# Performance work log

Hardware: AMD Instinct MI355X
Metric: run time of the kernel (lower is better)

The kernel has to match this reference:

```python
import jax, jax.numpy as jnp
import numpy as np

B, C, Ci, H, W = 8, 256, 128, 64, 64
EPS = 1e-5


def conv1x1(x, w, b):
    # x: [B,C,H,W], w: [O,C], b: [O] -> [B,O,H,W]
    return jnp.einsum('bchw,oc->bohw', x, w) + b[None, :, None, None]


def maxpool2(x):
    b, c, h, w = x.shape
    return x.reshape(b, c, h // 2, 2, w // 2, 2).max(axis=(3, 5))


def setup_inputs() -> dict:
    key = jax.random.key(0)
    ks = jax.random.split(key, 12)
    s_in = 1.0 / np.sqrt(C)
    s_ic = 1.0 / np.sqrt(Ci)
    return {
        'x': jax.random.normal(ks[0], (B, C, H, W), dtype=jnp.float32),
        'g_w': jax.random.normal(ks[1], (Ci, C), dtype=jnp.float32) * s_in,
        'g_b': jax.random.normal(ks[2], (Ci,), dtype=jnp.float32) * 0.01,
        'theta_w': jax.random.normal(ks[3], (Ci, C), dtype=jnp.float32) * s_in,
        'theta_b': jax.random.normal(ks[4], (Ci,), dtype=jnp.float32) * 0.01,
        'phi_w': jax.random.normal(ks[5], (Ci, C), dtype=jnp.float32) * s_in,
        'phi_b': jax.random.normal(ks[6], (Ci,), dtype=jnp.float32) * 0.01,
        'W_w': jax.random.normal(ks[7], (C, Ci), dtype=jnp.float32) * s_ic,
        'W_b': jax.random.normal(ks[8], (C,), dtype=jnp.float32) * 0.01,
        'bn_gamma': jax.random.normal(ks[9], (C,), dtype=jnp.float32) * 0.1 + 1.0,
        'bn_beta': jax.random.normal(ks[10], (C,), dtype=jnp.float32) * 0.1,
        'bn_mean': jnp.zeros((C,), dtype=jnp.float32),
        'bn_var': jax.random.uniform(ks[11], (C,), dtype=jnp.float32) * 0.5 + 0.75,
    }


def reference(x, g_w, g_b, theta_w, theta_b, phi_w, phi_b, W_w, W_b, bn_gamma, bn_beta, bn_mean, bn_var):
    b = x.shape[0]
    # g and phi: 1x1 conv then 2x2 max-pool (sub_sample=True)
    g_x = maxpool2(conv1x1(x, g_w, g_b)).reshape(b, Ci, -1)          # [B,Ci,Np]
    g_x = jnp.transpose(g_x, (0, 2, 1))                               # [B,Np,Ci]
    theta_x = conv1x1(x, theta_w, theta_b).reshape(b, Ci, -1)         # [B,Ci,N]
    theta_x = jnp.transpose(theta_x, (0, 2, 1))                       # [B,N,Ci]
    phi_x = maxpool2(conv1x1(x, phi_w, phi_b)).reshape(b, Ci, -1)     # [B,Ci,Np]
    f = jnp.einsum('bnc,bcm->bnm', theta_x, phi_x)                    # [B,N,Np]
    f_div_C = jax.nn.softmax(f, axis=-1)                              # embedded_gaussian: plain softmax, no scaling
    y = jnp.einsum('bnm,bmc->bnc', f_div_C, g_x)                      # [B,N,Ci]
    y = jnp.transpose(y, (0, 2, 1)).reshape(b, Ci, H, W)              # [B,Ci,H,W]
    # W: 1x1 conv + BatchNorm (inference form with running stats)
    W_y = conv1x1(y, W_w, W_b)
    inv = bn_gamma / jnp.sqrt(bn_var + EPS)
    W_y = (W_y - bn_mean[None, :, None, None]) * inv[None, :, None, None] + bn_beta[None, :, None, None]
    return W_y + x
```

## Files before the change

### kernel.cpp

```cpp
#include <hip/hip_runtime.h>
#include <math.h>

#define Bn   8
#define Cc   256
#define Cin  128
#define Hh   64
#define Ww   64
#define Nn   4096
#define Npl  1024
#define EPSf 1e-5f

typedef __attribute__((ext_vector_type(8))) short    short8;
typedef __attribute__((ext_vector_type(8))) _Float16 half8;
typedef __attribute__((ext_vector_type(4))) float    floatx4;

__device__ __forceinline__ unsigned short f2bf(float f) {
    unsigned int u = __float_as_uint(f);
    u += 0x7fffu + ((u >> 16) & 1u);
    return (unsigned short)(u >> 16);
}
__device__ __forceinline__ unsigned short f2h(float f) {
    _Float16 h = (_Float16)f;
    return __builtin_bit_cast(unsigned short, h);
}
__device__ __forceinline__ float h2f(unsigned short u) {
    return (float)__builtin_bit_cast(_Float16, u);
}

__device__ __forceinline__ unsigned int cvtpk_bf16(float lo, float hi) {
    unsigned int r;
    asm("v_cvt_pk_bf16_f32 %0, %1, %2" : "=v"(r) : "v"(lo), "v"(hi));
    return r;
}

__device__ __forceinline__ void gload_lds16(const unsigned short* g, unsigned short* l) {
    __builtin_amdgcn_global_load_lds(
        (const __attribute__((address_space(1))) unsigned int*)g,
        (__attribute__((address_space(3))) unsigned int*)l, 16, 0, 0);
}

__global__ __launch_bounds__(256) void k_prep(
    const float* __restrict__ g_w, const float* __restrict__ th_w,
    const float* __restrict__ ph_w,
    const float* __restrict__ W_w, const float* __restrict__ W_b,
    const float* __restrict__ gamma, const float* __restrict__ beta,
    const float* __restrict__ mean,  const float* __restrict__ var,
    unsigned short* __restrict__ gWh,
    unsigned short* __restrict__ thWh, unsigned short* __restrict__ thWl,
    unsigned short* __restrict__ phWh, unsigned short* __restrict__ phWl,
    unsigned short* __restrict__ Wh, float* __restrict__ cvec)
{
    int i = blockIdx.x * 256 + threadIdx.x;
    if (i < 98304) {
        int seg = i >> 15;
        int idx = i & 32767;
        float v = (seg == 0 ? g_w : (seg == 1 ? th_w : ph_w))[idx];
        unsigned short hi = f2h(v);
        if (seg == 0) gWh[idx] = hi;
        else {
            (seg == 1 ? thWh : phWh)[idx] = hi;
            (seg == 1 ? thWl : phWl)[idx] = f2h(v - h2f(hi));
        }
    } else {
        int j = i - 98304;
        int o = j >> 7;
        float inv = gamma[o] * rsqrtf(var[o] + EPSf);
        Wh[j] = f2h(W_w[j] * inv);
        if (j < Cc) {
            float invi = gamma[j] * rsqrtf(var[j] + EPSf);
            cvec[j] = (W_b[j] - mean[j]) * invi + beta[j];
        }
    }
}

#define XPAD 264

__global__ __launch_bounds__(256, 2) void k_conv3(
    const float* __restrict__ x,
    const unsigned short* __restrict__ gWh,
    const unsigned short* __restrict__ thWh, const unsigned short* __restrict__ thWl,
    const unsigned short* __restrict__ phWh, const unsigned short* __restrict__ phWl,
    const float* __restrict__ g_b, const float* __restrict__ th_b,
    const float* __restrict__ ph_b,
    unsigned short* __restrict__ thetaT,
    unsigned short* __restrict__ gPc,
    unsigned short* __restrict__ phiPt)
{
    __shared__ __align__(16) unsigned short Xhi[64 * XPAD];
    __shared__ __align__(16) unsigned short Xlo[64 * XPAD];

    const int t    = threadIdx.x;
    const int w    = t >> 6;
    const int l    = t & 63;
    const int quad = l >> 4;
    const int l16  = l & 15;
    const int b    = blockIdx.x >> 6;
    const int tile = blockIdx.x & 63;
    const int ty   = tile >> 1;
    const int tx   = tile & 1;

    {
        const float4* xg = (const float4*)x;
        unsigned int* XhiW = (unsigned int*)Xhi;
        unsigned int* XloW = (unsigned int*)Xlo;
        #pragma unroll
        for (int it = 0; it < 8; ++it) {
            int idx = t + 256 * it;
            int c2  = idx >> 4;
            int p4  = idx & 15;
            int n   = (2 * ty + (p4 >> 3)) * Ww + tx * 32 + (p4 & 7) * 4;
            float4 va = xg[((size_t)(b * Cc + 2 * c2) * Nn + n) >> 2];
            float4 vb = xg[((size_t)(b * Cc + 2 * c2 + 1) * Nn + n) >> 2];
            const float fa[4] = {va.x, va.y, va.z, va.w};
            const float fb[4] = {vb.x, vb.y, vb.z, vb.w};
            #pragma unroll
            for (int i = 0; i < 4; ++i) {
                int px = p4 * 4 + i;
                unsigned short ha = f2h(fa[i]), hb = f2h(fb[i]);
                unsigned short la = f2h(fa[i] - h2f(ha));
                unsigned short lb = f2h(fb[i] - h2f(hb));
                XhiW[px * 132 + c2] = (unsigned int)ha | ((unsigned int)hb << 16);
                XloW[px * 132 + c2] = (unsigned int)la | ((unsigned int)lb << 16);
            }
        }
    }
    __syncthreads();

    floatx4 acc[6][4] = {};

    #pragma unroll 2
    for (int kd = 0; kd < 8; ++kd) {
        half8 bhi[4], blo[4];
        #pragma unroll
        for (int nt = 0; nt < 4; ++nt) {
            bhi[nt] = *(const half8*)&Xhi[(nt * 16 + l16) * XPAD + kd * 32 + quad * 8];
            blo[nt] = *(const half8*)&Xlo[(nt * 16 + l16) * XPAD + kd * 32 + quad * 8];
        }
        #pragma unroll
        for (int ti = 0; ti < 6; ++ti) {
            int ot  = w + 4 * ti;
            int seg = ot >> 3;
            size_t aoff = (size_t)((ot & 7) * 16 + l16) * Cc + kd * 32 + quad * 8;
            const unsigned short* wh = (seg == 0 ? gWh : (seg == 1 ? thWh : phWh));
            half8 ah = *(const half8*)&wh[aoff];
            #pragma unroll
            for (int nt = 0; nt < 4; ++nt)
                acc[ti][nt] = __builtin_amdgcn_mfma_f32_16x16x32_f16(ah, bhi[nt], acc[ti][nt], 0, 0, 0);
            if (seg != 0) {
                const unsigned short* wl = (seg == 1 ? thWl : phWl);
                half8 al = *(const half8*)&wl[aoff];
                #pragma unroll
                for (int nt = 0; nt < 4; ++nt) {
                    acc[ti][nt] = __builtin_amdgcn_mfma_f32_16x16x32_f16(ah, blo[nt], acc[ti][nt], 0, 0, 0);
                    acc[ti][nt] = __builtin_amdgcn_mfma_f32_16x16x32_f16(al, bhi[nt], acc[ti][nt], 0, 0, 0);
                }
            }
        }
    }

    #pragma unroll
    for (int ti = 0; ti < 6; ++ti) {
        int ot  = w + 4 * ti;
        int seg = ot >> 3;
        int ol  = (ot & 7) * 16 + quad * 4;
        if (seg == 1) {
            float b0 = th_b[ol], b1 = th_b[ol + 1], b2 = th_b[ol + 2], b3 = th_b[ol + 3];
            #pragma unroll
            for (int nt = 0; nt < 4; ++nt) {
                int n = (2 * ty + (nt >> 1)) * Ww + tx * 32 + (nt & 1) * 16 + l16;
                ushort4 v;
                v.x = f2h(acc[ti][nt][0] + b0);
                v.y = f2h(acc[ti][nt][1] + b1);
                v.z = f2h(acc[ti][nt][2] + b2);
                v.w = f2h(acc[ti][nt][3] + b3);
                *(ushort4*)&thetaT[((size_t)b * Nn + n) * Cin + ol] = v;
            }
        } else {
            const float* bb = (seg == 0 ? g_b : ph_b);
            float b0 = bb[ol], b1 = bb[ol + 1], b2 = bb[ol + 2], b3 = bb[ol + 3];
            #pragma unroll
            for (int pp = 0; pp < 2; ++pp) {
                float pm[4];
                #pragma unroll
                for (int r = 0; r < 4; ++r) {
                    float m = fmaxf(acc[ti][pp][r], acc[ti][pp + 2][r]);
                    pm[r] = fmaxf(m, __shfl_xor(m, 1, 64));
                }
                int np = ty * 32 + tx * 16 + pp * 8 + (l16 >> 1);
                if ((l16 & 1) == 0) {
                    if (seg == 0) {
                        gPc[((size_t)b * Cin + ol + 0) * Npl + np] = f2bf(pm[0] + b0);
                        gPc[((size_t)b * Cin + ol + 1) * Npl + np] = f2bf(pm[1] + b1);
                        gPc[((size_t)b * Cin + ol + 2) * Npl + np] = f2bf(pm[2] + b2);
                        gPc[((size_t)b * Cin + ol + 3) * Npl + np] = f2bf(pm[3] + b3);
                    } else {
                        ushort4 v;
                        v.x = f2h(pm[0] + b0); v.y = f2h(pm[1] + b1);
                        v.z = f2h(pm[2] + b2); v.w = f2h(pm[3] + b3);
                        *(ushort4*)&phiPt[((size_t)b * Npl + np) * Cin + ol] = v;
                    }
                }
            }
        }
    }
}

__device__ __forceinline__ void stage_kv(
    unsigned short* smem, int sel, int chg, int b, int grp, int wq,
    int mK, int gK, int cV, int gV,
    const unsigned short* __restrict__ phiPt,
    const unsigned short* __restrict__ gPc)
{
    unsigned short* Kb = smem + sel * 16384;
    if (grp == 0) {
        #pragma unroll
        for (int j = 0; j < 4; ++j) {
            int slot = wq * 4 + j;
            int m  = slot * 4 + mK;
            int gs = gK ^ (m & 7);
            gload_lds16(&phiPt[((size_t)b * Npl + chg * 64 + m) * Cin + gs * 8],
                        &Kb[slot * 512]);
        }
    } else {
        unsigned short* Vb = Kb + 8192;
        #pragma unroll
        for (int j = 0; j < 4; ++j) {
            int slot = wq * 4 + j;
            int c  = slot * 8 + cV;
            int gs = gV ^ (c & 7);
            gload_lds16(&gPc[((size_t)b * Cin + c) * Npl + chg * 64 + gs * 8],
                        &Vb[slot * 512]);
        }
    }
}

#define SSHIFT 20.0f

__global__ __launch_bounds__(512, 4) void k_attn_out(
    const unsigned short* __restrict__ thetaT,
    const unsigned short* __restrict__ phiPt,
    const unsigned short* __restrict__ gPc,
    const unsigned short* __restrict__ Wh,
    const float* __restrict__ cvec,
    const float* __restrict__ x,
    float* __restrict__ out)
{
    __shared__ __align__(16) unsigned short smem[40960];

    const int t    = threadIdx.x;
    const int w    = t >> 6;
    const int wq   = w & 3;
    const int grp  = w >> 2;
    const int l    = t & 63;
    const int quad = l >> 4;
    const int l16  = l & 15;
    const int bid  = blockIdx.x;
    const int wid  = (bid & 7) * 64 + (bid >> 3);
    const int b    = wid >> 6;
    const int qb   = wid & 63;
    const int n0   = qb * 64;

    uint4 qr[4];
    #pragma unroll
    for (int kd = 0; kd < 4; ++kd)
        qr[kd] = *(const uint4*)&thetaT[((size_t)b * Nn + n0 + wq * 16 + l16) * Cin
                                        + kd * 32 + quad * 8];
    #pragma unroll
    for (int kd = 0; kd < 4; ++kd)
        asm volatile("" : "+v"(qr[kd].x), "+v"(qr[kd].y), "+v"(qr[kd].z), "+v"(qr[kd].w));
    half8 qf[4];
    #pragma unroll
    for (int kd = 0; kd < 4; ++kd) qf[kd] = __builtin_bit_cast(half8, qr[kd]);

    floatx4 yacc[8] = {};
    float liq = 0.f;

    const int mK = l >> 4;
    const int gK = l & 15;
    const int cV = l >> 3;
    const int gV = l & 7;

    stage_kv(smem, 0, 0, b, grp, wq, mK, gK, cV, gV, phiPt, gPc);
    asm volatile("s_waitcnt vmcnt(0)" ::: "memory");
    __syncthreads();

    #pragma unroll 2
    for (int ch = 0; ch < 16; ++ch) {
        const int cur = ch & 1;
        if (ch < 15)
            stage_kv(smem, cur ^ 1, ch + 1, b, grp, wq, mK, gK, cV, gV, phiPt, gPc);

        const unsigned short* Ks = smem + cur * 16384;
        const unsigned short* Vt = Ks + 8192;

        floatx4 sacc[2] = {};
        #pragma unroll
        for (int mtl = 0; mtl < 2; ++mtl) {
            int mt = grp * 2 + mtl;
            #pragma unroll
            for (int kd = 0; kd < 4; ++kd) {
                half8 kf = *(const half8*)&Ks[(mt * 16 + l16) * 128
                                              + (((kd * 4 + quad) ^ (l16 & 7)) << 3)];
                sacc[mtl] = __builtin_amdgcn_mfma_f32_16x16x32_f16(kf, qf[kd], sacc[mtl], 0, 0, 0);
            }
        }

        float ex0[4], ex1[4];
        #pragma unroll
        for (int r = 0; r < 4; ++r) {
            ex0[r] = __expf(sacc[0][r] - SSHIFT);
            ex1[r] = __expf(sacc[1][r] - SSHIFT);
            liq += ex0[r] + ex1[r];
        }

        unsigned int a0 = cvtpk_bf16(ex0[0], ex0[1]);
        unsigned int a1 = cvtpk_bf16(ex1[0], ex1[1]);
        unsigned int b0 = cvtpk_bf16(ex0[2], ex0[3]);
        unsigned int b1 = cvtpk_bf16(ex1[2], ex1[3]);
        asm volatile("v_permlane32_swap_b32 %0, %1" : "+v"(a0), "+v"(a1));
        asm volatile("v_permlane16_swap_b32 %0, %1" : "+v"(a0), "+v"(a1));
        asm volatile("v_permlane32_swap_b32 %0, %1" : "+v"(b0), "+v"(b1));
        asm volatile("v_permlane16_swap_b32 %0, %1" : "+v"(b0), "+v"(b1));
        uint4 pw; pw.x = a0; pw.y = b0; pw.z = a1; pw.w = b1;
        short8 pf = __builtin_bit_cast(short8, pw);

        #pragma unroll
        for (int ct = 0; ct < 8; ++ct) {
            short8 vf = *(const short8*)&Vt[(ct * 16 + l16) * 64
                                            + (((grp * 4 + quad) ^ (l16 & 7)) << 3)];
            yacc[ct] = __builtin_amdgcn_mfma_f32_16x16x32_bf16(pf, vf, yacc[ct], 0, 0, 0);
        }

        asm volatile("s_waitcnt vmcnt(0)" ::: "memory");
        __syncthreads();
    }

    liq += __shfl_xor(liq, 16, 64);
    liq += __shfl_xor(liq, 32, 64);

    float* cbuf = (float*)smem;
    const int ci = (wq * 64 + l) * 33;
    if (grp == 1) {
        #pragma unroll
        for (int ct = 0; ct < 8; ++ct)
            #pragma unroll
            for (int r = 0; r < 4; ++r) cbuf[ci + ct * 4 + r] = yacc[ct][r];
        cbuf[ci + 32] = liq;
    }
    __syncthreads();
    if (grp == 0) {
        #pragma unroll
        for (int ct = 0; ct < 8; ++ct)
            #pragma unroll
            for (int r = 0; r < 4; ++r) yacc[ct][r] += cbuf[ci + ct * 4 + r];
        liq += cbuf[ci + 32];
    }
    __syncthreads();

    {
        unsigned short* Ws = smem + 8192;
        #pragma unroll
        for (int j = 0; j < 8; ++j) {
            int slot = w * 8 + j;
            int row  = slot * 4 + mK;
            int gs   = gK ^ (row & 7);
            gload_lds16(&Wh[(size_t)row * Cin + gs * 8], &Ws[slot * 512]);
        }
    }

    if (grp == 0) {
        unsigned int* Yw = (unsigned int*)smem;
        #pragma unroll
        for (int r = 0; r < 4; ++r) {
            float lr = __shfl(liq, quad * 4 + r, 64);
            float il = 1.0f / lr;
            int q  = wq * 16 + quad * 4 + r;
            int q7 = q & 7;
            #pragma unroll
            for (int ct = 0; ct < 8; ++ct) {
                unsigned int h = f2h(yacc[ct][r] * il);
                unsigned int p = (unsigned int)__shfl_xor((int)h, 1, 64);
                if ((l16 & 1) == 0) {
                    int g = ct * 2 + (l16 >> 3);
                    Yw[q * 64 + (((g ^ q7) << 2) | ((l16 & 7) >> 1))] = h | (p << 16);
                }
            }
        }
    }
    asm volatile("s_waitcnt vmcnt(0)" ::: "memory");
    __syncthreads();

    const unsigned short* Ys = smem;
    const unsigned short* Ws = smem + 8192;

    half8 af[2][4];
    #pragma unroll
    for (int mt = 0; mt < 2; ++mt)
        #pragma unroll
        for (int kd = 0; kd < 4; ++kd) {
            int row = w * 32 + mt * 16 + l16;
            af[mt][kd] = *(const half8*)&Ws[row * 128
                                            + (((kd * 4 + quad) ^ (l16 & 7)) << 3)];
        }

    floatx4 acc[2][4] = {};
    #pragma unroll
    for (int nt = 0; nt < 4; ++nt) {
        half8 bfr[4];
        #pragma unroll
        for (int kd = 0; kd < 4; ++kd)
            bfr[kd] = *(const half8*)&Ys[(nt * 16 + l16) * 128
                                         + (((kd * 4 + quad) ^ (l16 & 7)) << 3)];
        #pragma unroll
        for (int mt = 0; mt < 2; ++mt)
            #pragma unroll
            for (int kd = 0; kd < 4; ++kd)
                acc[mt][nt] = __builtin_amdgcn_mfma_f32_16x16x32_f16(af[mt][kd], bfr[kd], acc[mt][nt], 0, 0, 0);
    }

    #pragma unroll
    for (int mt = 0; mt < 2; ++mt) {
        #pragma unroll
        for (int r = 0; r < 4; ++r) {
            int o = w * 32 + mt * 16 + quad * 4 + r;
            float cv = cvec[o];
            #pragma unroll
            for (int nt = 0; nt < 4; ++nt) {
                size_t gi = ((size_t)(b * Cc + o)) * Nn + n0 + nt * 16 + l16;
                out[gi] = acc[mt][nt][r] + cv + x[gi];
            }
        }
    }
}

extern "C" void kernel_launch(void* const* d_in, const int* in_sizes, int n_in,
                              void* d_out, int out_size, void* d_ws, size_t ws_size,
                              hipStream_t stream) {
    const float* x    = (const float*)d_in[0];
    const float* g_w  = (const float*)d_in[1];
    const float* g_b  = (const float*)d_in[2];
    const float* th_w = (const float*)d_in[3];
    const float* th_b = (const float*)d_in[4];
    const float* ph_w = (const float*)d_in[5];
    const float* ph_b = (const float*)d_in[6];
    const float* W_w  = (const float*)d_in[7];
    const float* W_b  = (const float*)d_in[8];
    const float* gmm  = (const float*)d_in[9];
    const float* bta  = (const float*)d_in[10];
    const float* mmn  = (const float*)d_in[11];
    const float* vvr  = (const float*)d_in[12];
    float* out = (float*)d_out;

    unsigned short* thetaT = (unsigned short*)d_ws;
    unsigned short* phiPt  = thetaT + (size_t)4194304;
    unsigned short* gPc    = phiPt + (size_t)1048576;
    unsigned short* Wh     = gPc + (size_t)1048576;
    unsigned short* gWh    = Wh + 32768;
    unsigned short* thWh   = gWh + 32768;
    unsigned short* thWl   = thWh + 32768;
    unsigned short* phWh   = thWl + 32768;
    unsigned short* phWl   = phWh + 32768;
    float*          cvec   = (float*)(phWl + 32768);

    k_prep<<<dim3(512), dim3(256), 0, stream>>>(
        g_w, th_w, ph_w, W_w, W_b, gmm, bta, mmn, vvr,
        gWh, thWh, thWl, phWh, phWl, Wh, cvec);
    k_conv3<<<dim3(Bn * 64), dim3(256), 0, stream>>>(
        x, gWh, thWh, thWl, phWh, phWl, g_b, th_b, ph_b, thetaT, gPc, phiPt);
    k_attn_out<<<dim3(Bn * 64), dim3(512), 0, stream>>>(
        thetaT, phiPt, gPc, Wh, cvec, x, out);
}
```

Baseline: 165.7 us.

## Stream V fragments from global to registers and ring-buffer K in LDS

The attention loop no longer stages V (g) tiles through LDS. Each wave now loads its V MFMA fragments straight from global memory into registers. K tiles move to a 4-slot LDS ring that is prefetched three chunks ahead and guarded by partial vmcnt waits with plain s_barrier instead of full drains, and the output-projection weights are also read directly from global into registers. This cuts LDS footprint and traffic and removes the full vmcnt(0)+syncthreads per chunk, at the cost of more uncoalesced global loads and higher register pressure.

```diff
diff --git a/kernel.cpp b/kernel.cpp
--- a/kernel.cpp
+++ b/kernel.cpp
@@ -205,35 +205,6 @@
     }
 }
 
-__device__ __forceinline__ void stage_kv(
-    unsigned short* smem, int sel, int chg, int b, int grp, int wq,
-    int mK, int gK, int cV, int gV,
-    const unsigned short* __restrict__ phiPt,
-    const unsigned short* __restrict__ gPc)
-{
-    unsigned short* Kb = smem + sel * 16384;
-    if (grp == 0) {
-        #pragma unroll
-        for (int j = 0; j < 4; ++j) {
-            int slot = wq * 4 + j;
-            int m  = slot * 4 + mK;
-            int gs = gK ^ (m & 7);
-            gload_lds16(&phiPt[((size_t)b * Npl + chg * 64 + m) * Cin + gs * 8],
-                        &Kb[slot * 512]);
-        }
-    } else {
-        unsigned short* Vb = Kb + 8192;
-        #pragma unroll
-        for (int j = 0; j < 4; ++j) {
-            int slot = wq * 4 + j;
-            int c  = slot * 8 + cV;
-            int gs = gV ^ (c & 7);
-            gload_lds16(&gPc[((size_t)b * Cin + c) * Npl + chg * 64 + gs * 8],
-                        &Vb[slot * 512]);
-        }
-    }
-}
-
 #define SSHIFT 20.0f
 
 __global__ __launch_bounds__(512, 4) void k_attn_out(
@@ -245,7 +216,7 @@
     const float* __restrict__ x,
     float* __restrict__ out)
 {
-    __shared__ __align__(16) unsigned short smem[40960];
+    __shared__ __align__(16) unsigned short smem[32768];
 
     const int t    = threadIdx.x;
     const int w    = t >> 6;
@@ -277,21 +248,43 @@
 
     const int mK = l >> 4;
     const int gK = l & 15;
-    const int cV = l >> 3;
-    const int gV = l & 7;
-
-    stage_kv(smem, 0, 0, b, grp, wq, mK, gK, cV, gV, phiPt, gPc);
-    asm volatile("s_waitcnt vmcnt(0)" ::: "memory");
-    __syncthreads();
-
-    #pragma unroll 2
+
+    #pragma unroll
+    for (int pc = 0; pc < 3; ++pc) {
+        unsigned short* Kb = smem + pc * 8192;
+        #pragma unroll
+        for (int j = 0; j < 2; ++j) {
+            int slot = w * 2 + j;
+            int m  = slot * 4 + mK;
+            int gs = gK ^ (m & 7);
+            gload_lds16(&phiPt[((size_t)b * Npl + pc * 64 + m) * Cin + gs * 8],
+                        &Kb[slot * 512]);
+        }
+    }
+    asm volatile("s_waitcnt vmcnt(4)" ::: "memory");
+    __builtin_amdgcn_s_barrier();
+
     for (int ch = 0; ch < 16; ++ch) {
-        const int cur = ch & 1;
-        if (ch < 15)
-            stage_kv(smem, cur ^ 1, ch + 1, b, grp, wq, mK, gK, cV, gV, phiPt, gPc);
-
-        const unsigned short* Ks = smem + cur * 16384;
-        const unsigned short* Vt = Ks + 8192;
+        short8 vf[8];
+        #pragma unroll
+        for (int ct = 0; ct < 8; ++ct)
+            vf[ct] = *(const short8*)&gPc[((size_t)b * Cin + ct * 16 + l16) * Npl
+                                          + ch * 64 + grp * 32 + quad * 8];
+        __builtin_amdgcn_sched_barrier(0);
+
+        if (ch < 13) {
+            unsigned short* Kb = smem + ((ch + 3) & 3) * 8192;
+            #pragma unroll
+            for (int j = 0; j < 2; ++j) {
+                int slot = w * 2 + j;
+                int m  = slot * 4 + mK;
+                int gs = gK ^ (m & 7);
+                gload_lds16(&phiPt[((size_t)b * Npl + (ch + 3) * 64 + m) * Cin + gs * 8],
+                            &Kb[slot * 512]);
+            }
+        }
+
+        const unsigned short* Ks = smem + (ch & 3) * 8192;
 
         floatx4 sacc[2] = {};
         #pragma unroll
@@ -325,14 +318,10 @@
         short8 pf = __builtin_bit_cast(short8, pw);
 
         #pragma unroll
-        for (int ct = 0; ct < 8; ++ct) {
-            short8 vf = *(const short8*)&Vt[(ct * 16 + l16) * 64
-                                            + (((grp * 4 + quad) ^ (l16 & 7)) << 3)];
-            yacc[ct] = __builtin_amdgcn_mfma_f32_16x16x32_bf16(pf, vf, yacc[ct], 0, 0, 0);
-        }
-
-        asm volatile("s_waitcnt vmcnt(0)" ::: "memory");
-        __syncthreads();
+        for (int ct = 0; ct < 8; ++ct)
+            yacc[ct] = __builtin_amdgcn_mfma_f32_16x16x32_bf16(pf, vf[ct], yacc[ct], 0, 0, 0);
+
+        __builtin_amdgcn_s_barrier();
     }
 
     liq += __shfl_xor(liq, 16, 64);
@@ -357,16 +346,13 @@
     }
     __syncthreads();
 
-    {
-        unsigned short* Ws = smem + 8192;
-        #pragma unroll
-        for (int j = 0; j < 8; ++j) {
-            int slot = w * 8 + j;
-            int row  = slot * 4 + mK;
-            int gs   = gK ^ (row & 7);
-            gload_lds16(&Wh[(size_t)row * Cin + gs * 8], &Ws[slot * 512]);
-        }
-    }
+    half8 af[2][4];
+    #pragma unroll
+    for (int mt = 0; mt < 2; ++mt)
+        #pragma unroll
+        for (int kd = 0; kd < 4; ++kd)
+            af[mt][kd] = *(const half8*)&Wh[(size_t)(w * 32 + mt * 16 + l16) * Cin
+                                            + kd * 32 + quad * 8];
 
     if (grp == 0) {
         unsigned int* Yw = (unsigned int*)smem;
@@ -387,21 +373,9 @@
             }
         }
     }
-    asm volatile("s_waitcnt vmcnt(0)" ::: "memory");
     __syncthreads();
 
     const unsigned short* Ys = smem;
-    const unsigned short* Ws = smem + 8192;
-
-    half8 af[2][4];
-    #pragma unroll
-    for (int mt = 0; mt < 2; ++mt)
-        #pragma unroll
-        for (int kd = 0; kd < 4; ++kd) {
-            int row = w * 32 + mt * 16 + l16;
-            af[mt][kd] = *(const half8*)&Ws[row * 128
-                                            + (((kd * 4 + quad) ^ (l16 & 7)) << 3)];
-        }
 
     floatx4 acc[2][4] = {};
     #pragma unroll
```

Result: slower. 204.0 us (+23.1%).
